# Kernel optimization log

Hardware: AMD Instinct MI355X
Metric: run time of the kernel (lower is better)

Reference implementation:

```python
import jax, jax.numpy as jnp
import numpy as np

N = 20000   # nodes
E = 40000   # directed edges
F_IN = 13   # dataset.num_features
G = 1000    # graphs in batch
DIMS = [(13, 32), (32, 64), (64, 64)]  # (M_in, M_out) per NNConv layer


def setup_inputs() -> dict:
    key = jax.random.key(0)
    ks = list(jax.random.split(key, 32))
    inp = {}
    inp["x"] = jax.random.normal(ks[0], (N, F_IN), jnp.float32)
    inp["edge_index"] = jax.random.randint(ks[1], (2, E), 0, N, dtype=jnp.int32)
    inp["edge_attr"] = jax.random.uniform(ks[2], (E, 5), dtype=jnp.float32)
    inp["batch"] = jnp.sort(jax.random.randint(ks[3], (N,), 0, G, dtype=jnp.int32))
    i = 4
    for l, (mi, mo) in enumerate(DIMS):
        inp[f"w1_{l}"] = jax.random.normal(ks[i], (5, 128), jnp.float32) / np.sqrt(5.0).astype(np.float32); i += 1
        inp[f"b1_{l}"] = jnp.zeros((128,), jnp.float32)
        inp[f"w2_{l}"] = jax.random.normal(ks[i], (128, mi * mo), jnp.float32) / np.sqrt(128.0).astype(np.float32); i += 1
        inp[f"b2_{l}"] = jnp.zeros((mi * mo,), jnp.float32)
        inp[f"root_{l}"] = jax.random.normal(ks[i], (mi, mo), jnp.float32) / np.sqrt(float(mi)).astype(np.float32); i += 1
        inp[f"bias_{l}"] = jnp.zeros((mo,), jnp.float32)
    inp["fc1_w"] = jax.random.normal(ks[i], (64, 32), jnp.float32) / 8.0; i += 1
    inp["fc1_b"] = jnp.zeros((32,), jnp.float32)
    inp["fc2_w"] = jax.random.normal(ks[i], (32, 16), jnp.float32) / np.sqrt(32.0).astype(np.float32); i += 1
    inp["fc2_b"] = jnp.zeros((16,), jnp.float32)
    inp["fc3_w"] = jax.random.normal(ks[i], (16, 1), jnp.float32) / 4.0; i += 1
    inp["fc3_b"] = jnp.zeros((1,), jnp.float32)
    return inp


def _nnconv(x, src, dst, edge_attr, w1, b1, w2, b2, root, bias, mi, mo):
    # edge MLP: [E,5] -> [E,128] -> [E, mi*mo] per-edge weight matrices
    h = jax.nn.relu(edge_attr @ w1 + b1)
    We = (h @ w2 + b2).reshape(-1, mi, mo)          # [E, mi, mo]
    msg = jnp.einsum('ei,eio->eo', x[src], We)      # gather + per-edge matmul
    agg = jax.ops.segment_sum(msg, dst, num_segments=x.shape[0])  # scatter-add
    return x @ root + agg + bias                    # NNConv root weight + bias


def _forward(x, edge_index, edge_attr, batch, convs, fc1_w, fc1_b, fc2_w, fc2_b, fc3_w, fc3_b):
    src, dst = edge_index[0], edge_index[1]
    for (mi, mo), (w1, b1, w2, b2, root, bias) in zip(DIMS, convs):
        x = jax.nn.elu(_nnconv(x, src, dst, edge_attr, w1, b1, w2, b2, root, bias, mi, mo))
    # scatter_mean pooling over graphs
    sums = jax.ops.segment_sum(x, batch, num_segments=G)
    cnt = jax.ops.segment_sum(jnp.ones((x.shape[0],), x.dtype), batch, num_segments=G)
    xg = sums / jnp.maximum(cnt, 1.0)[:, None]
    xg = jax.nn.elu(xg @ fc1_w + fc1_b)
    xg = jax.nn.elu(xg @ fc2_w + fc2_b)
    return (xg @ fc3_w + fc3_b).reshape(-1)


def reference(x, edge_index, edge_attr, batch,
              w1_0, b1_0, w2_0, b2_0, root_0, bias_0,
              w1_1, b1_1, w2_1, b2_1, root_1, bias_1,
              w1_2, b1_2, w2_2, b2_2, root_2, bias_2,
              fc1_w, fc1_b, fc2_w, fc2_b, fc3_w, fc3_b):
    convs = [(w1_0, b1_0, w2_0, b2_0, root_0, bias_0),
             (w1_1, b1_1, w2_1, b2_1, root_1, bias_1),
             (w1_2, b1_2, w2_2, b2_2, root_2, bias_2)]
    return _forward(x, edge_index, edge_attr, batch, convs,
                    fc1_w, fc1_b, fc2_w, fc2_b, fc3_w, fc3_b)
```

## Files before the change

### kernel.cpp

```cpp
#include <hip/hip_runtime.h>
#include <stdint.h>
#include <math.h>

typedef _Float16 half8_t __attribute__((ext_vector_type(8)));
typedef float floatx4 __attribute__((ext_vector_type(4)));

#define NN 20000
#define NE 40000
#define NG 1000
#define NBLK 313
#define NSPLIT 4

__global__ __launch_bounds__(256) void prep_fused_kernel(
    const float* __restrict__ x, _Float16* __restrict__ e16,
    const float* __restrict__ w2a, const float* __restrict__ b2a, _Float16* __restrict__ oa,
    const float* __restrict__ w2b, const float* __restrict__ b2b, _Float16* __restrict__ ob,
    const float* __restrict__ w2c, const float* __restrict__ b2c, _Float16* __restrict__ oc,
    int* __restrict__ deg)
{
  if (blockIdx.x < 1250) {
    int idx = blockIdx.x * 256 + threadIdx.x;
    int n = idx >> 4, i = idx & 15;
    e16[idx] = (i < 13) ? (_Float16)x[(size_t)n * 13 + i] : (_Float16)0.f;
    return;
  }
  if (blockIdx.x >= 1680) {
    int n = (blockIdx.x - 1680) * 256 + threadIdx.x;
    if (n < NN) deg[n] = 0;
    return;
  }
  const int TOT0 = 68 * 2 * 64, TOT1 = 132 * 4 * 64, TOT2 = 264 * 4 * 64;
  int idx = (blockIdx.x - 1250) * 256 + threadIdx.x;
  const float *w2, *b2; _Float16* op; int mi, mo, mpsh, CT;
  if (idx < TOT0) { w2 = w2a; b2 = b2a; op = oa; mi = 13; mo = 32; mpsh = 4; CT = 2; }
  else if (idx < TOT0 + TOT1) { idx -= TOT0; w2 = w2b; b2 = b2b; op = ob; mi = 32; mo = 64; mpsh = 5; CT = 4; }
  else if (idx < TOT0 + TOT1 + TOT2) { idx -= TOT0 + TOT1; w2 = w2c; b2 = b2c; op = oc; mi = 64; mo = 64; mpsh = 6; CT = 4; }
  else return;
  int l = idx & 63;
  int ct = (idx >> 6) % CT;
  int c = idx / (64 * CT);
  int q = l >> 4;
  int n = ct * 16 + (l & 15);
  int mask = (1 << mpsh) - 1;
  half8_t v;
#pragma unroll
  for (int j = 0; j < 8; ++j) {
    int r = c * 32 + q * 8 + j;
    int k = r >> mpsh, i = r & mask;
    float f = 0.f;
    if (i < mi) {
      if (k < 128) f = w2[(size_t)(k * mi + i) * mo + n];
      else if (k == 128) f = b2[(size_t)i * mo + n];
    }
    v[j] = (_Float16)f;
  }
  *(half8_t*)(op + (size_t)idx * 8) = v;
}

__global__ __launch_bounds__(256) void deg_kernel(const int* __restrict__ dst, int* __restrict__ deg) {
  int e = blockIdx.x * 256 + threadIdx.x;
  if (e < NE) atomicAdd(&deg[dst[e]], 1);
}

__global__ __launch_bounds__(1024) void scan_kernel(
    const int* __restrict__ deg, int* __restrict__ row_ptr, int* __restrict__ cursor)
{
  constexpr int CH = 20;
  __shared__ int wsum[16];
  int t = threadIdx.x;
  int lane = t & 63, w = t >> 6;
  int base = t * CH;
  int local[CH];
#pragma unroll
  for (int i = 0; i < CH; ++i) {
    int n = base + i;
    local[i] = (n < NN) ? deg[n] : 0;
  }
  int s = 0;
#pragma unroll
  for (int i = 0; i < CH; ++i) s += local[i];
  int sc = s;
#pragma unroll
  for (int d = 1; d < 64; d <<= 1) {
    int v = __shfl_up(sc, d, 64);
    if (lane >= d) sc += v;
  }
  if (lane == 63) wsum[w] = sc;
  __syncthreads();
  if (w == 0 && lane < 16) {
    int v = wsum[lane];
    int scc = v;
#pragma unroll
    for (int d = 1; d < 16; d <<= 1) {
      int u = __shfl_up(scc, d, 64);
      if (lane >= d) scc += u;
    }
    wsum[lane] = scc - v;
  }
  __syncthreads();
  int run = wsum[w] + (sc - s);
#pragma unroll
  for (int i = 0; i < CH; ++i) {
    int n = base + i;
    if (n < NN) { row_ptr[n] = run; cursor[n] = run; run += local[i]; }
    else if (n == NN) row_ptr[NN] = run;
  }
}

__global__ __launch_bounds__(256) void fill_kernel(
    const int* __restrict__ dst, int* __restrict__ cursor, int* __restrict__ eids)
{
  int e = blockIdx.x * 256 + threadIdx.x;
  if (e < NE) { int p = atomicAdd(&cursor[dst[e]], 1); eids[p] = e; }
}

template <int MIP, int MO, int NCC, int KCNT>
__global__ __launch_bounds__(256, 4) void msg9_kernel(
    const float* __restrict__ ea, const float* __restrict__ w1,
    const float* __restrict__ b1, const _Float16* __restrict__ xe,
    const int* __restrict__ src,
    const _Float16* __restrict__ w2h, _Float16* __restrict__ msgp)
{
  constexpr int EPB = 128;
  constexpr int CT = MO / 16;
  constexpr int CHB = CT * 1024;
  constexpr int XV = (MIP == 64) ? 2 : 1;
  constexpr int KH = (KCNT + 1) >> 1;

  __shared__ uint4 wsb[2][CHB / 16];
  __shared__ _Float16 h16[KCNT * EPB];
  __shared__ float w1s[5 * 128 + 128];

  const int t = threadIdx.x;
  const int wave = t >> 6, lane = t & 63;
  const int l15 = lane & 15, q = lane >> 4;
  const int split = blockIdx.x / NBLK;
  const int e0 = (blockIdx.x % NBLK) * EPB;
  const int c0 = NCC * split;
  const int kg0 = KCNT * split;

  const char* wgp = (const char*)w2h + (size_t)c0 * CHB;
  uint4 ra4, rb4; uint2 ra2, rb2;
  if constexpr (CT == 4) {
    ra4 = *(const uint4*)(wgp + t * 16);
    rb4 = *(const uint4*)(wgp + CHB + t * 16);
  } else {
    ra2 = *(const uint2*)(wgp + t * 8);
    rb2 = *(const uint2*)(wgp + CHB + t * 8);
  }

  const int wbase = wave * 32;
  half8_t xf[2][XV];
#pragma unroll
  for (int s = 0; s < 2; ++s) {
    int eg = e0 + wbase + s * 16 + l15; if (eg >= NE) eg = NE - 1;
    const _Float16* xr = xe + (size_t)src[eg] * MIP;
    int i0 = (MIP == 16) ? (q & 1) * 8 : q * 8;
    xf[s][0] = *(const half8_t*)(xr + i0);
    if constexpr (MIP == 64)
      xf[s][XV - 1] = *(const half8_t*)(xr + 32 + q * 8);
  }

  const int te = t & 127;
  float ear[5];
  {
    int eg = e0 + te; if (eg >= NE) eg = NE - 1;
#pragma unroll
    for (int j = 0; j < 5; ++j) ear[j] = ea[(size_t)eg * 5 + j];
  }
  for (int i = t; i < 768; i += 256) w1s[i] = (i < 640) ? w1[i] : b1[i - 640];
  __syncthreads();

  {
    int kh = t >> 7;
    int klo = kh * KH;
    int khi = klo + KH; if (khi > KCNT) khi = KCNT;
    for (int kl = klo; kl < khi; ++kl) {
      int kg = kg0 + kl;
      float v;
      if (kg < 128) {
        v = w1s[640 + kg];
#pragma unroll
        for (int j = 0; j < 5; ++j) v = fmaf(ear[j], w1s[j * 128 + kg], v);
        v = fmaxf(v, 0.f);
      } else v = (kg == 128) ? 1.f : 0.f;
      h16[kl * EPB + te] = (_Float16)v;
    }
  }
  __syncthreads();

  floatx4 acc[2][CT];
#pragma unroll
  for (int s = 0; s < 2; ++s)
#pragma unroll
    for (int b = 0; b < CT; ++b) acc[s][b] = (floatx4){0.f, 0.f, 0.f, 0.f};

#pragma unroll 2
  for (int cc = 0; cc < NCC; ++cc) {
    const bool odd = (cc & 1) != 0;
    if constexpr (CT == 4) wsb[cc & 1][t] = odd ? rb4 : ra4;
    else ((uint2*)wsb[cc & 1])[t] = odd ? rb2 : ra2;
    if (cc + 2 < NCC) {
      const char* np = wgp + (size_t)(cc + 2) * CHB;
      if constexpr (CT == 4) {
        if (odd) rb4 = *(const uint4*)(np + t * 16); else ra4 = *(const uint4*)(np + t * 16);
      } else {
        if (odd) rb2 = *(const uint2*)(np + t * 8); else ra2 = *(const uint2*)(np + t * 8);
      }
    }
    __syncthreads();
    const _Float16* wb = (const _Float16*)wsb[cc & 1];
    half8_t bf[CT];
#pragma unroll
    for (int b = 0; b < CT; ++b)
      bf[b] = *(const half8_t*)(wb + (b * 64 + lane) * 8);
    int kl;
    if constexpr (MIP == 64) kl = cc >> 1;
    else if constexpr (MIP == 32) kl = cc;
    else kl = 2 * cc + (q >> 1);
#pragma unroll
    for (int s = 0; s < 2; ++s) {
      _Float16 hv = h16[kl * EPB + wbase + s * 16 + l15];
      half8_t af;
      if constexpr (MIP == 64) af = xf[s][cc & 1] * hv;
      else af = xf[s][0] * hv;
#pragma unroll
      for (int b = 0; b < CT; ++b)
        acc[s][b] = __builtin_amdgcn_mfma_f32_16x16x32_f16(af, bf[b], acc[s][b], 0, 0, 0);
    }
  }

  _Float16* mp = msgp + (size_t)split * NE * MO;
#pragma unroll
  for (int s = 0; s < 2; ++s) {
    int rowb = wbase + s * 16 + q * 4;
#pragma unroll
    for (int b = 0; b < CT; ++b) {
      int n = b * 16 + l15;
#pragma unroll
      for (int r = 0; r < 4; ++r) {
        int row = rowb + r;
        int e = e0 + row;
        if (e < NE) mp[(size_t)e * MO + n] = (_Float16)acc[s][b][r];
      }
    }
  }
}

template <int MIP, int NCC, int KCNT>
__global__ __launch_bounds__(256, 3) void msgN_kernel(
    const float* __restrict__ ea, const float* __restrict__ w1,
    const float* __restrict__ b1, const _Float16* __restrict__ xe,
    const int* __restrict__ src,
    const _Float16* __restrict__ w2h, _Float16* __restrict__ msgp)
{
  constexpr int EPB = 128;
  constexpr int MO = 64;
  constexpr int CT = 4;
  constexpr int CHB = CT * 1024;
  constexpr int XV = (MIP == 64) ? 2 : 1;
  constexpr int KH = (KCNT + 1) >> 1;
  constexpr int NG8 = KCNT / 8;
  constexpr int JT = KCNT % 8;
  constexpr int NGT = (KCNT + 7) / 8;

  __shared__ _Float16 h16[NGT * EPB * 8];
  __shared__ float w1s[5 * 128 + 128];

  const int t = threadIdx.x;
  const int wave = t >> 6, lane = t & 63;
  const int l15 = lane & 15, q = lane >> 4;
  const int split = blockIdx.x / NBLK;
  const int e0 = (blockIdx.x % NBLK) * EPB;
  const int c0 = NCC * split;
  const int kg0 = KCNT * split;
  const char* wgp = (const char*)w2h + (size_t)c0 * CHB;

  const int te = t & 127;
  float ear[5];
  {
    int eg = e0 + te; if (eg >= NE) eg = NE - 1;
#pragma unroll
    for (int j = 0; j < 5; ++j) ear[j] = ea[(size_t)eg * 5 + j];
  }
  for (int i = t; i < 768; i += 256) w1s[i] = (i < 640) ? w1[i] : b1[i - 640];
  __syncthreads();

  {
    int kh = t >> 7;
    int klo = kh * KH;
    int khi = klo + KH; if (khi > KCNT) khi = KCNT;
    for (int kl = klo; kl < khi; ++kl) {
      int kg = kg0 + kl;
      float v;
      if (kg < 128) {
        v = w1s[640 + kg];
#pragma unroll
        for (int j = 0; j < 5; ++j) v = fmaf(ear[j], w1s[j * 128 + kg], v);
        v = fmaxf(v, 0.f);
      } else v = (kg == 128) ? 1.f : 0.f;
      h16[((kl >> 3) * EPB + te) * 8 + (kl & 7)] = (_Float16)v;
    }
  }
  __syncthreads();

  half8_t xf[8][XV];
#pragma unroll
  for (int m = 0; m < 8; ++m) {
    int eg = e0 + m * 16 + l15; if (eg >= NE) eg = NE - 1;
    const _Float16* xr = xe + (size_t)src[eg] * MIP;
    xf[m][0] = *(const half8_t*)(xr + q * 8);
    if constexpr (MIP == 64)
      xf[m][XV - 1] = *(const half8_t*)(xr + 32 + q * 8);
  }

  floatx4 acc[8];
#pragma unroll
  for (int m = 0; m < 8; ++m) acc[m] = (floatx4){0.f, 0.f, 0.f, 0.f};

  const char* wq = wgp + (size_t)wave * 1024 + (size_t)lane * 16;

#pragma unroll
  for (int g = 0; g < NGT; ++g) {
    half8_t h8[8];
#pragma unroll
    for (int m = 0; m < 8; ++m)
      h8[m] = *(const half8_t*)(h16 + ((size_t)g * EPB + m * 16 + l15) * 8);
    const int jn = (g < NG8) ? 8 : JT;
#pragma unroll
    for (int j = 0; j < 8; ++j) {
      if (j < jn) {
        const int kl = g * 8 + j;
        if constexpr (MIP == 64) {
#pragma unroll
          for (int hf = 0; hf < 2; ++hf) {
            const int cc = kl * 2 + hf;
            half8_t bf = *(const half8_t*)(wq + (size_t)cc * CHB);
#pragma unroll
            for (int m = 0; m < 8; ++m) {
              half8_t af = xf[m][hf] * h8[m][j];
              acc[m] = __builtin_amdgcn_mfma_f32_16x16x32_f16(af, bf, acc[m], 0, 0, 0);
            }
          }
        } else {
          const int cc = kl;
          half8_t bf = *(const half8_t*)(wq + (size_t)cc * CHB);
#pragma unroll
          for (int m = 0; m < 8; ++m) {
            half8_t af = xf[m][0] * h8[m][j];
            acc[m] = __builtin_amdgcn_mfma_f32_16x16x32_f16(af, bf, acc[m], 0, 0, 0);
          }
        }
      }
    }
  }

  _Float16* mp = msgp + (size_t)split * NE * MO;
  const int n = wave * 16 + l15;
#pragma unroll
  for (int m = 0; m < 8; ++m) {
    int rowb = m * 16 + q * 4;
#pragma unroll
    for (int r = 0; r < 4; ++r) {
      int e = e0 + rowb + r;
      if (e < NE) mp[(size_t)e * MO + n] = (_Float16)acc[m][r];
    }
  }
}

template <int MIN_, int XST, int MO, int FINAL>
__global__ __launch_bounds__(256) void gather_kernel(
    const _Float16* __restrict__ e16in, const float* __restrict__ root,
    const float* __restrict__ bias, const int* __restrict__ row_ptr,
    const int* __restrict__ eids, const _Float16* __restrict__ msgp,
    _Float16* __restrict__ oute, float* __restrict__ outf)
{
  constexpr int NPB = 256 / MO;
  int n = blockIdx.x * NPB + threadIdx.x / MO;
  int o = threadIdx.x % MO;
  if (n >= NN) return;
  float a = bias[o];
#pragma unroll
  for (int i = 0; i < MIN_; ++i)
    a = fmaf((float)e16in[(size_t)n * XST + i], root[i * MO + o], a);
  int r0 = row_ptr[n], r1 = row_ptr[n + 1];
  for (int j = r0; j < r1; ++j) {
    int e = eids[j];
#pragma unroll
    for (int s = 0; s < NSPLIT; ++s)
      a += (float)msgp[((size_t)s * NE + e) * MO + o];
  }
  if constexpr (FINAL) {
    outf[(size_t)n * MO + o] = a;
  } else {
    float v = a > 0.f ? a : (expf(a) - 1.f);
    oute[(size_t)n * MO + o] = (_Float16)v;
  }
}

__global__ __launch_bounds__(64) void pool_fc_kernel(
    const float* __restrict__ xn2, const int* __restrict__ batch,
    const float* __restrict__ f1w, const float* __restrict__ f1b,
    const float* __restrict__ f2w, const float* __restrict__ f2b,
    const float* __restrict__ f3w, const float* __restrict__ f3b,
    float* __restrict__ out)
{
  __shared__ float xg[64]; __shared__ float a1[32]; __shared__ float a2[16];
  int g = blockIdx.x, t = threadIdx.x;
  int lo = 0, hi = NN;
  while (lo < hi) { int m = (lo + hi) >> 1; if (batch[m] < g) lo = m + 1; else hi = m; }
  int start = lo; hi = NN;
  while (lo < hi) { int m = (lo + hi) >> 1; if (batch[m] <= g) lo = m + 1; else hi = m; }
  int end = lo;
  float acc = 0.f;
  for (int n = start; n < end; ++n) {
    float v = xn2[(size_t)n * 64 + t];
    acc += v > 0.f ? v : (expf(v) - 1.f);
  }
  float c = (end > start) ? (float)(end - start) : 1.f;
  xg[t] = acc / c;
  __syncthreads();
  if (t < 32) {
    float a = f1b[t];
    for (int i = 0; i < 64; ++i) a = fmaf(xg[i], f1w[i * 32 + t], a);
    a1[t] = a > 0.f ? a : (expf(a) - 1.f);
  }
  __syncthreads();
  if (t < 16) {
    float a = f2b[t];
    for (int i = 0; i < 32; ++i) a = fmaf(a1[i], f2w[i * 16 + t], a);
    a2[t] = a > 0.f ? a : (expf(a) - 1.f);
  }
  __syncthreads();
  if (t == 0) {
    float a = f3b[0];
    for (int i = 0; i < 16; ++i) a = fmaf(a2[i], f3w[i], a);
    out[g] = a;
  }
}

extern "C" void kernel_launch(void* const* d_in, const int* in_sizes, int n_in,
                              void* d_out, int out_size, void* d_ws, size_t ws_size,
                              hipStream_t stream)
{
  const float* x_in  = (const float*)d_in[0];
  const int*   ei    = (const int*)d_in[1];
  const float* ea    = (const float*)d_in[2];
  const int*   batch = (const int*)d_in[3];
  const float* W1[3] = {(const float*)d_in[4],  (const float*)d_in[10], (const float*)d_in[16]};
  const float* B1[3] = {(const float*)d_in[5],  (const float*)d_in[11], (const float*)d_in[17]};
  const float* W2[3] = {(const float*)d_in[6],  (const float*)d_in[12], (const float*)d_in[18]};
  const float* B2[3] = {(const float*)d_in[7],  (const float*)d_in[13], (const float*)d_in[19]};
  const float* RT[3] = {(const float*)d_in[8],  (const float*)d_in[14], (const float*)d_in[20]};
  const float* BS[3] = {(const float*)d_in[9],  (const float*)d_in[15], (const float*)d_in[21]};
  const float* f1w = (const float*)d_in[22]; const float* f1b = (const float*)d_in[23];
  const float* f2w = (const float*)d_in[24]; const float* f2b = (const float*)d_in[25];
  const float* f3w = (const float*)d_in[26]; const float* f3b = (const float*)d_in[27];

  char* ws = (char*)d_ws;
  size_t off = 0;
  auto alloc = [&](size_t bytes) { void* p = ws + off; off += (bytes + 255) & ~(size_t)255; return p; };
  float*    xn2   = (float*)alloc((size_t)NN * 64 * 4);
  _Float16* e16_0 = (_Float16*)alloc((size_t)NN * 16 * 2);
  _Float16* e16_1 = (_Float16*)alloc((size_t)NN * 32 * 2);
  _Float16* e16_2 = (_Float16*)alloc((size_t)NN * 64 * 2);
  _Float16* w2h0  = (_Float16*)alloc((size_t)68 * 2048);
  _Float16* w2h1  = (_Float16*)alloc((size_t)132 * 4096);
  _Float16* w2h2  = (_Float16*)alloc((size_t)264 * 4096);
  _Float16* msgp  = (_Float16*)alloc((size_t)NSPLIT * NE * 64 * 2);
  int*      deg     = (int*)alloc((size_t)NN * 4);
  int*      row_ptr = (int*)alloc((size_t)(NN + 1) * 4);
  int*      cursor  = (int*)alloc((size_t)NN * 4);
  int*      eids    = (int*)alloc((size_t)NE * 4);

  const int* srcp = ei;
  const int* dstp = ei + NE;

  prep_fused_kernel<<<1680 + (NN + 255) / 256, 256, 0, stream>>>(
      x_in, e16_0, W2[0], B2[0], w2h0, W2[1], B2[1], w2h1, W2[2], B2[2], w2h2, deg);
  deg_kernel<<<(NE + 255) / 256, 256, 0, stream>>>(dstp, deg);
  scan_kernel<<<1, 1024, 0, stream>>>(deg, row_ptr, cursor);
  fill_kernel<<<(NE + 255) / 256, 256, 0, stream>>>(dstp, cursor, eids);

  msg9_kernel<16, 32, 17, 34><<<NBLK * NSPLIT, 256, 0, stream>>>(
      ea, W1[0], B1[0], e16_0, srcp, w2h0, msgp);
  gather_kernel<13, 16, 32, 0><<<(NN + 7) / 8, 256, 0, stream>>>(
      e16_0, RT[0], BS[0], row_ptr, eids, msgp, e16_1, xn2);

  msgN_kernel<32, 33, 33><<<NBLK * NSPLIT, 256, 0, stream>>>(
      ea, W1[1], B1[1], e16_1, srcp, w2h1, msgp);
  gather_kernel<32, 32, 64, 0><<<(NN + 3) / 4, 256, 0, stream>>>(
      e16_1, RT[1], BS[1], row_ptr, eids, msgp, e16_2, xn2);

  msgN_kernel<64, 66, 33><<<NBLK * NSPLIT, 256, 0, stream>>>(
      ea, W1[2], B1[2], e16_2, srcp, w2h2, msgp);
  gather_kernel<64, 64, 64, 1><<<(NN + 3) / 4, 256, 0, stream>>>(
      e16_2, RT[2], BS[2], row_ptr, eids, msgp, e16_2, xn2);

  pool_fc_kernel<<<NG, 64, 0, stream>>>(xn2, batch, f1w, f1b, f2w, f2b, f3w, f3b, (float*)d_out);
}
```

Measured before the change: 306.9 us.

## Stage edge-MLP weight chunks in double-buffered LDS with 2x2 wave tiling

The layer-2/3 message kernel now splits its tile into a 2x2 wave grid (64 edges by 32 outputs per wave) instead of each wave owning 16 output columns for all 128 edges. Each W2 chunk is loaded cooperatively into a double-buffered LDS slot, with register prefetch two chunks ahead, instead of every wave reading its slice straight from global memory. The h16 layout changes to per-k rows and the occupancy hint rises from 3 to 4 blocks per CU. The aim is to cut global weight traffic and register pressure, at the cost of one block barrier per chunk.

New measurement: 297.5 us. 1.03x faster.

```diff
diff --git a/kernel.cpp b/kernel.cpp
--- a/kernel.cpp
+++ b/kernel.cpp
@@ -248,7 +248,7 @@
 }
 
 template <int MIP, int NCC, int KCNT>
-__global__ __launch_bounds__(256, 3) void msgN_kernel(
+__global__ __launch_bounds__(256, 4) void msgH_kernel(
     const float* __restrict__ ea, const float* __restrict__ w1,
     const float* __restrict__ b1, const _Float16* __restrict__ xe,
     const int* __restrict__ src,
@@ -256,25 +256,37 @@
 {
   constexpr int EPB = 128;
   constexpr int MO = 64;
-  constexpr int CT = 4;
-  constexpr int CHB = CT * 1024;
+  constexpr int CHB = 4096;
   constexpr int XV = (MIP == 64) ? 2 : 1;
   constexpr int KH = (KCNT + 1) >> 1;
-  constexpr int NG8 = KCNT / 8;
-  constexpr int JT = KCNT % 8;
-  constexpr int NGT = (KCNT + 7) / 8;
-
-  __shared__ _Float16 h16[NGT * EPB * 8];
+
+  __shared__ uint4 wsb[2][CHB / 16];
+  __shared__ _Float16 h16[KCNT * EPB];
   __shared__ float w1s[5 * 128 + 128];
 
   const int t = threadIdx.x;
   const int wave = t >> 6, lane = t & 63;
   const int l15 = lane & 15, q = lane >> 4;
+  const int mw = wave >> 1;
+  const int nw = wave & 1;
   const int split = blockIdx.x / NBLK;
   const int e0 = (blockIdx.x % NBLK) * EPB;
   const int c0 = NCC * split;
   const int kg0 = KCNT * split;
+
   const char* wgp = (const char*)w2h + (size_t)c0 * CHB;
+  uint4 ra4 = *(const uint4*)(wgp + t * 16);
+  uint4 rb4 = *(const uint4*)(wgp + CHB + t * 16);
+
+  half8_t xf[4][XV];
+#pragma unroll
+  for (int s = 0; s < 4; ++s) {
+    int eg = e0 + mw * 64 + s * 16 + l15; if (eg >= NE) eg = NE - 1;
+    const _Float16* xr = xe + (size_t)src[eg] * MIP;
+    xf[s][0] = *(const half8_t*)(xr + q * 8);
+    if constexpr (MIP == 64)
+      xf[s][XV - 1] = *(const half8_t*)(xr + 32 + q * 8);
+  }
 
   const int te = t & 127;
   float ear[5];
@@ -299,71 +311,58 @@
         for (int j = 0; j < 5; ++j) v = fmaf(ear[j], w1s[j * 128 + kg], v);
         v = fmaxf(v, 0.f);
       } else v = (kg == 128) ? 1.f : 0.f;
-      h16[((kl >> 3) * EPB + te) * 8 + (kl & 7)] = (_Float16)v;
-    }
-  }
-  __syncthreads();
-
-  half8_t xf[8][XV];
-#pragma unroll
-  for (int m = 0; m < 8; ++m) {
-    int eg = e0 + m * 16 + l15; if (eg >= NE) eg = NE - 1;
-    const _Float16* xr = xe + (size_t)src[eg] * MIP;
-    xf[m][0] = *(const half8_t*)(xr + q * 8);
-    if constexpr (MIP == 64)
-      xf[m][XV - 1] = *(const half8_t*)(xr + 32 + q * 8);
-  }
-
-  floatx4 acc[8];
-#pragma unroll
-  for (int m = 0; m < 8; ++m) acc[m] = (floatx4){0.f, 0.f, 0.f, 0.f};
-
-  const char* wq = wgp + (size_t)wave * 1024 + (size_t)lane * 16;
-
-#pragma unroll
-  for (int g = 0; g < NGT; ++g) {
-    half8_t h8[8];
-#pragma unroll
-    for (int m = 0; m < 8; ++m)
-      h8[m] = *(const half8_t*)(h16 + ((size_t)g * EPB + m * 16 + l15) * 8);
-    const int jn = (g < NG8) ? 8 : JT;
-#pragma unroll
-    for (int j = 0; j < 8; ++j) {
-      if (j < jn) {
-        const int kl = g * 8 + j;
-        if constexpr (MIP == 64) {
-#pragma unroll
-          for (int hf = 0; hf < 2; ++hf) {
-            const int cc = kl * 2 + hf;
-            half8_t bf = *(const half8_t*)(wq + (size_t)cc * CHB);
-#pragma unroll
-            for (int m = 0; m < 8; ++m) {
-              half8_t af = xf[m][hf] * h8[m][j];
-              acc[m] = __builtin_amdgcn_mfma_f32_16x16x32_f16(af, bf, acc[m], 0, 0, 0);
-            }
-          }
-        } else {
-          const int cc = kl;
-          half8_t bf = *(const half8_t*)(wq + (size_t)cc * CHB);
-#pragma unroll
-          for (int m = 0; m < 8; ++m) {
-            half8_t af = xf[m][0] * h8[m][j];
-            acc[m] = __builtin_amdgcn_mfma_f32_16x16x32_f16(af, bf, acc[m], 0, 0, 0);
-          }
-        }
+      h16[kl * EPB + te] = (_Float16)v;
+    }
+  }
+  __syncthreads();
+
+  floatx4 acc[4][2];
+#pragma unroll
+  for (int s = 0; s < 4; ++s)
+#pragma unroll
+    for (int b = 0; b < 2; ++b) acc[s][b] = (floatx4){0.f, 0.f, 0.f, 0.f};
+
+#pragma unroll 2
+  for (int cc = 0; cc < NCC; ++cc) {
+    const bool odd = (cc & 1) != 0;
+    wsb[cc & 1][t] = odd ? rb4 : ra4;
+    if (cc + 2 < NCC) {
+      const char* np = wgp + (size_t)(cc + 2) * CHB;
+      if (odd) rb4 = *(const uint4*)(np + t * 16); else ra4 = *(const uint4*)(np + t * 16);
+    }
+    __syncthreads();
+    const _Float16* wb = (const _Float16*)wsb[cc & 1];
+    half8_t bf[2];
+#pragma unroll
+    for (int b = 0; b < 2; ++b)
+      bf[b] = *(const half8_t*)(wb + ((nw * 2 + b) * 64 + lane) * 8);
+    int kl;
+    if constexpr (MIP == 64) kl = cc >> 1;
+    else kl = cc;
+#pragma unroll
+    for (int s = 0; s < 4; ++s) {
+      _Float16 hv = h16[kl * EPB + mw * 64 + s * 16 + l15];
+      half8_t af;
+      if constexpr (MIP == 64) af = xf[s][cc & 1] * hv;
+      else af = xf[s][0] * hv;
+#pragma unroll
+      for (int b = 0; b < 2; ++b)
+        acc[s][b] = __builtin_amdgcn_mfma_f32_16x16x32_f16(af, bf[b], acc[s][b], 0, 0, 0);
+    }
+  }
+
+  _Float16* mp = msgp + (size_t)split * NE * MO;
+#pragma unroll
+  for (int s = 0; s < 4; ++s) {
+    int rowb = mw * 64 + s * 16 + q * 4;
+#pragma unroll
+    for (int b = 0; b < 2; ++b) {
+      int n = nw * 32 + b * 16 + l15;
+#pragma unroll
+      for (int r = 0; r < 4; ++r) {
+        int e = e0 + rowb + r;
+        if (e < NE) mp[(size_t)e * MO + n] = (_Float16)acc[s][b][r];
       }
-    }
-  }
-
-  _Float16* mp = msgp + (size_t)split * NE * MO;
-  const int n = wave * 16 + l15;
-#pragma unroll
-  for (int m = 0; m < 8; ++m) {
-    int rowb = m * 16 + q * 4;
-#pragma unroll
-    for (int r = 0; r < 4; ++r) {
-      int e = e0 + rowb + r;
-      if (e < NE) mp[(size_t)e * MO + n] = (_Float16)acc[m][r];
     }
   }
 }
@@ -487,12 +486,12 @@
   gather_kernel<13, 16, 32, 0><<<(NN + 7) / 8, 256, 0, stream>>>(
       e16_0, RT[0], BS[0], row_ptr, eids, msgp, e16_1, xn2);
 
-  msgN_kernel<32, 33, 33><<<NBLK * NSPLIT, 256, 0, stream>>>(
+  msgH_kernel<32, 33, 33><<<NBLK * NSPLIT, 256, 0, stream>>>(
       ea, W1[1], B1[1], e16_1, srcp, w2h1, msgp);
   gather_kernel<32, 32, 64, 0><<<(NN + 3) / 4, 256, 0, stream>>>(
       e16_1, RT[1], BS[1], row_ptr, eids, msgp, e16_2, xn2);
 
-  msgN_kernel<64, 66, 33><<<NBLK * NSPLIT, 256, 0, stream>>>(
+  msgH_kernel<64, 66, 33><<<NBLK * NSPLIT, 256, 0, stream>>>(
       ea, W1[2], B1[2], e16_2, srcp, w2h2, msgp);
   gather_kernel<64, 64, 64, 1><<<(NN + 3) / 4, 256, 0, stream>>>(
       e16_2, RT[2], BS[2], row_ptr, eids, msgp, e16_2, xn2);
```
